# Performance work log

Hardware: AMD Instinct MI355X
Metric: run time of the kernel (lower is better)

Reference implementation:

```python
import jax, jax.numpy as jnp
import numpy as np

# YOLOv1 loss constants (from init_kwargs)
S, B, C = 28, 2, 20
L_COORD, L_NOOBJ = 5.0, 0.5
LEN_PRED = 5 * B + C  # 30
BS = 512


def setup_inputs() -> dict:
    key = jax.random.key(0)
    k1, k2, k3 = jax.random.split(key, 3)
    prediction = jax.random.uniform(k1, (BS, S, S, LEN_PRED), dtype=jnp.float32)
    target = jax.random.uniform(k2, (BS, S, S, LEN_PRED), dtype=jnp.float32)
    obj = jax.random.bernoulli(k3, 0.05, (BS, S, S)).astype(jnp.float32)
    idx = jnp.arange(LEN_PRED)
    is_conf = (idx < 5 * B) & (idx % 5 == 4)
    target = jnp.where(is_conf, obj[..., None], target)
    return {"prediction": prediction, "target": target}


def _xyxy(box):
    # [x, y, w, h] (cell-relative center, image-relative wh) -> [x1, y1, x2, y2]
    xy = box[..., :2] / S
    wh = box[..., 2:4]
    return xy - 0.5 * wh, xy + 0.5 * wh


def reference(prediction, target):
    N = prediction.shape[0]
    dt = prediction.dtype
    coo = (target[..., 4] > 0).astype(dt)   # (bs,S,S) cells with an object
    noo = 1.0 - coo                          # cells without an object

    pb = prediction[..., :5 * B].reshape(prediction.shape[:3] + (B, 5))  # (bs,S,S,B,5)
    tb = target[..., :5 * B].reshape(target.shape[:3] + (B, 5))

    # IoU of each predicted box vs the (single) target box of the cell
    p_lt, p_rb = _xyxy(pb)                 # (bs,S,S,B,2)
    t_lt, t_rb = _xyxy(tb[..., 0, :])      # (bs,S,S,2)
    lt = jnp.maximum(p_lt, t_lt[..., None, :])
    rb = jnp.minimum(p_rb, t_rb[..., None, :])
    wh = jnp.clip(rb - lt, 0.0)
    inter = wh[..., 0] * wh[..., 1]        # (bs,S,S,B)
    area1 = jnp.prod(p_rb - p_lt, axis=-1)
    area2 = jnp.prod(t_rb - t_lt, axis=-1)[..., None]
    iou = jax.lax.stop_gradient(inter / (area1 + area2 - inter))  # .data in torch

    max_idx = jnp.argmax(iou, axis=-1)     # responsible box per cell
    max_iou = jnp.max(iou, axis=-1)
    resp = jax.nn.one_hot(max_idx, B, dtype=dt)    # (bs,S,S,B)
    w_resp = coo[..., None] * resp                  # responsible & object
    w_not = coo[..., None] * (1.0 - resp)           # not responsible & object

    # Term 1+2: location loss (xy MSE + sqrt-wh MSE) on responsible boxes
    d_xy = jnp.sum((pb[..., :2] - tb[..., :2]) ** 2, axis=-1)
    d_wh = jnp.sum((jnp.sqrt(pb[..., 2:4]) - jnp.sqrt(tb[..., 2:4])) ** 2, axis=-1)
    loc_loss = jnp.sum(w_resp * (d_xy + d_wh))

    contain_loss = jnp.sum(w_resp * (pb[..., 4] - max_iou[..., None]) ** 2)

    # Term 4a: not-responsible boxes in object cells -> confidence target 0
    not_response_loss = jnp.sum(w_not * pb[..., 4] ** 2)

    # Term 4b: confidence loss in no-object cells (all B boxes)
    nooobj_loss = jnp.sum(noo[..., None] * (pb[..., 4] - tb[..., 4]) ** 2)

    # Term 5: class MSE in object cells
    class_loss = jnp.sum(coo[..., None] * (prediction[..., 5 * B:] - target[..., 5 * B:]) ** 2)

    loss = (L_COORD * loc_loss + contain_loss
            + L_NOOBJ * (not_response_loss + nooobj_loss) + class_loss)
    return loss / N
```

## Files before the change

### kernel.cpp

```cpp
#include <hip/hip_runtime.h>

namespace {
constexpr int   kS          = 28;
constexpr int   kBatch      = 512;
constexpr int   kCells      = kBatch * kS * kS;
constexpr int   kTPB        = 256;
constexpr int   kTileCells  = 256;
constexpr int   kTileF      = kTileCells * 30;
constexpr int   kNBlocks    = kCells / kTileCells;
constexpr int   kChunks     = kTileF / (64 * 4);
constexpr float kLCoord     = 5.0f;
constexpr float kLNoobj     = 0.5f;
constexpr float kInvS       = 1.0f / 28.0f;
constexpr float kInvN       = 1.0f / 512.0f;
}

__device__ __forceinline__ void async16(const float* g, float* l) {
    __builtin_amdgcn_global_load_lds(
        (const __attribute__((address_space(1))) void*)g,
        (__attribute__((address_space(3))) void*)l,
        16, 0, 0);
}

__device__ __forceinline__ float cell_loss(const float* p, const float* t) {
    const float coo = (t[4] > 0.0f) ? 1.0f : 0.0f;

    const float t_cx = t[0] * kInvS, t_cy = t[1] * kInvS;
    const float t_ltx = t_cx - 0.5f * t[2];
    const float t_lty = t_cy - 0.5f * t[3];
    const float t_rbx = t_cx + 0.5f * t[2];
    const float t_rby = t_cy + 0.5f * t[3];
    const float area2 = (t_rbx - t_ltx) * (t_rby - t_lty);

    float iou0 = 0.0f, iou1 = 0.0f;
    #pragma unroll
    for (int b = 0; b < 2; ++b) {
        const float* pb = p + 5 * b;
        const float p_cx = pb[0] * kInvS, p_cy = pb[1] * kInvS;
        const float p_ltx = p_cx - 0.5f * pb[2];
        const float p_lty = p_cy - 0.5f * pb[3];
        const float p_rbx = p_cx + 0.5f * pb[2];
        const float p_rby = p_cy + 0.5f * pb[3];
        const float ltx = fmaxf(p_ltx, t_ltx);
        const float lty = fmaxf(p_lty, t_lty);
        const float rbx = fminf(p_rbx, t_rbx);
        const float rby = fminf(p_rby, t_rby);
        const float w = fmaxf(rbx - ltx, 0.0f);
        const float h = fmaxf(rby - lty, 0.0f);
        const float inter = w * h;
        const float area1 = (p_rbx - p_ltx) * (p_rby - p_lty);
        const float iou = inter / (area1 + area2 - inter);
        if (b == 0) iou0 = iou; else iou1 = iou;
    }
    const int   max_idx = (iou1 > iou0) ? 1 : 0;
    const float max_iou = fmaxf(iou0, iou1);

    float loc = 0.0f, contain = 0.0f, notresp = 0.0f, nooobj = 0.0f;
    #pragma unroll
    for (int b = 0; b < 2; ++b) {
        const float* pb = p + 5 * b;
        const float* tb = t + 5 * b;
        const float dx = pb[0] - tb[0];
        const float dy = pb[1] - tb[1];
        const float d_xy = dx * dx + dy * dy;
        const float sw = sqrtf(pb[2]) - sqrtf(tb[2]);
        const float sh = sqrtf(pb[3]) - sqrtf(tb[3]);
        const float d_wh = sw * sw + sh * sh;
        const float resp   = (b == max_idx) ? 1.0f : 0.0f;
        const float w_resp = coo * resp;
        const float w_not  = coo * (1.0f - resp);
        loc += w_resp * (d_xy + d_wh);
        const float dc = pb[4] - max_iou;
        contain += w_resp * dc * dc;
        notresp += w_not * pb[4] * pb[4];
        const float dn = pb[4] - tb[4];
        nooobj += (1.0f - coo) * dn * dn;
    }

    float cls = 0.0f;
    #pragma unroll
    for (int j = 10; j < 30; ++j) {
        const float d = p[j] - t[j];
        cls += d * d;
    }
    cls *= coo;

    return kLCoord * loc + contain + kLNoobj * (notresp + nooobj) + cls;
}

template <bool USE_WS>
__global__ __launch_bounds__(kTPB) void yolo_loss_kernel(
        const float* __restrict__ pred,
        const float* __restrict__ targ,
        float* __restrict__ dst) {
    __shared__ float lp[kTileF];
    __shared__ float lt[kTileF];
    __shared__ float wsum[kTPB / 64];

    const int tid  = threadIdx.x;
    const int lane = tid & 63;
    const int wid  = tid >> 6;

    const float* gp = pred + (size_t)blockIdx.x * kTileF;
    const float* gt = targ + (size_t)blockIdx.x * kTileF;

    for (int c = wid; c < kChunks; c += kTPB / 64) {
        const int f = c * 256 + lane * 4;
        async16(gp + f, &lp[c * 256]);
        async16(gt + f, &lt[c * 256]);
    }
    __syncthreads();

    float local = cell_loss(&lp[tid * 30], &lt[tid * 30]);

    #pragma unroll
    for (int off = 32; off > 0; off >>= 1)
        local += __shfl_down(local, off, 64);

    if (lane == 0) wsum[wid] = local;
    __syncthreads();
    if (tid == 0) {
        const float s = wsum[0] + wsum[1] + wsum[2] + wsum[3];
        if (USE_WS) dst[blockIdx.x] = s;
        else        atomicAdd(dst, s * kInvN);
    }
}

__global__ __launch_bounds__(256) void reduce_kernel(
        const float* __restrict__ part, float* __restrict__ out) {
    __shared__ float wsum[4];
    float s = 0.0f;
    for (int i = threadIdx.x; i < kNBlocks; i += 256) s += part[i];
    #pragma unroll
    for (int off = 32; off > 0; off >>= 1)
        s += __shfl_down(s, off, 64);
    const int lane = threadIdx.x & 63;
    const int wid  = threadIdx.x >> 6;
    if (lane == 0) wsum[wid] = s;
    __syncthreads();
    if (threadIdx.x == 0)
        out[0] = (wsum[0] + wsum[1] + wsum[2] + wsum[3]) * kInvN;
}

__global__ void zero_out_kernel(float* __restrict__ out) {
    if (threadIdx.x == 0) out[0] = 0.0f;
}

extern "C" void kernel_launch(void* const* d_in, const int* in_sizes, int n_in,
                              void* d_out, int out_size, void* d_ws, size_t ws_size,
                              hipStream_t stream) {
    const float* pred = (const float*)d_in[0];
    const float* targ = (const float*)d_in[1];
    float* out = (float*)d_out;

    if (ws_size >= (size_t)kNBlocks * sizeof(float)) {
        float* part = (float*)d_ws;
        yolo_loss_kernel<true><<<kNBlocks, kTPB, 0, stream>>>(pred, targ, part);
        reduce_kernel<<<1, 256, 0, stream>>>(part, out);
    } else {
        zero_out_kernel<<<1, 64, 0, stream>>>(out);
        yolo_loss_kernel<false><<<kNBlocks, kTPB, 0, stream>>>(pred, targ, out);
    }
}
```

Measured before the change: 23.04 us.

## Use persistent 512-block grid with double-buffered async LDS staging

```diff
diff --git a/kernel.cpp b/kernel.cpp
--- a/kernel.cpp
+++ b/kernel.cpp
@@ -1,18 +1,17 @@
 #include <hip/hip_runtime.h>
 
 namespace {
-constexpr int   kS          = 28;
-constexpr int   kBatch      = 512;
-constexpr int   kCells      = kBatch * kS * kS;
-constexpr int   kTPB        = 256;
-constexpr int   kTileCells  = 256;
-constexpr int   kTileF      = kTileCells * 30;
-constexpr int   kNBlocks    = kCells / kTileCells;
-constexpr int   kChunks     = kTileF / (64 * 4);
-constexpr float kLCoord     = 5.0f;
-constexpr float kLNoobj     = 0.5f;
-constexpr float kInvS       = 1.0f / 28.0f;
-constexpr float kInvN       = 1.0f / 512.0f;
+constexpr int   kCells     = 512 * 28 * 28;
+constexpr int   kHalfCells = 128;
+constexpr int   kHalfF     = kHalfCells * 30;
+constexpr int   kNHalves   = kCells / kHalfCells;
+constexpr int   kNBlk      = 512;
+constexpr int   kBaseH     = kNHalves / kNBlk;
+constexpr int   kExtra     = kNHalves % kNBlk;
+constexpr float kLCoord    = 5.0f;
+constexpr float kLNoobj    = 0.5f;
+constexpr float kInvS      = 1.0f / 28.0f;
+constexpr float kInvN      = 1.0f / 512.0f;
 }
 
 __device__ __forceinline__ void async16(const float* g, float* l) {
@@ -21,6 +20,8 @@
         (__attribute__((address_space(3))) void*)l,
         16, 0, 0);
 }
+__device__ __forceinline__ void wait_vm15() { asm volatile("s_waitcnt vmcnt(15)" ::: "memory"); }
+__device__ __forceinline__ void wait_vm0()  { asm volatile("s_waitcnt vmcnt(0)"  ::: "memory"); }
 
 __device__ __forceinline__ float cell_loss(const float* p, const float* t) {
     const float coo = (t[4] > 0.0f) ? 1.0f : 0.0f;
@@ -89,39 +90,57 @@
 }
 
 template <bool USE_WS>
-__global__ __launch_bounds__(kTPB) void yolo_loss_kernel(
+__global__ __launch_bounds__(128) void yolo_loss_kernel(
         const float* __restrict__ pred,
         const float* __restrict__ targ,
         float* __restrict__ dst) {
-    __shared__ float lp[kTileF];
-    __shared__ float lt[kTileF];
-    __shared__ float wsum[kTPB / 64];
+    __shared__ float lp[2][kHalfF];
+    __shared__ float lt[2][kHalfF];
+    __shared__ float wsum[2];
 
     const int tid  = threadIdx.x;
     const int lane = tid & 63;
     const int wid  = tid >> 6;
+    const int b    = blockIdx.x;
 
-    const float* gp = pred + (size_t)blockIdx.x * kTileF;
-    const float* gt = targ + (size_t)blockIdx.x * kTileF;
+    const int h0 = b * kBaseH + min(b, kExtra);
+    const int H  = kBaseH + (b < kExtra ? 1 : 0);
 
-    for (int c = wid; c < kChunks; c += kTPB / 64) {
-        const int f = c * 256 + lane * 4;
-        async16(gp + f, &lp[c * 256]);
-        async16(gt + f, &lt[c * 256]);
+    const float* gsrc = (wid == 0) ? pred : targ;
+
+    auto stage = [&](int h, int buf) {
+        const float* g = gsrc + (size_t)h * kHalfF;
+        float* l = (wid == 0) ? &lp[buf][0] : &lt[buf][0];
+        #pragma unroll
+        for (int c = 0; c < 15; ++c) {
+            const int f = c * 256 + lane * 4;
+            async16(g + f, l + c * 256);
+        }
+    };
+
+    stage(h0, 0);
+    if (H > 1) stage(h0 + 1, 1);
+
+    float acc = 0.0f;
+    for (int i = 0; i < H; ++i) {
+        const int buf = i & 1;
+        if (i + 1 < H) wait_vm15(); else wait_vm0();
+        __builtin_amdgcn_s_barrier();
+        acc += cell_loss(&lp[buf][tid * 30], &lt[buf][tid * 30]);
+        if (i + 2 < H) {
+            __builtin_amdgcn_s_barrier();
+            stage(h0 + i + 2, buf);
+        }
     }
-    __syncthreads();
-
-    float local = cell_loss(&lp[tid * 30], &lt[tid * 30]);
 
     #pragma unroll
     for (int off = 32; off > 0; off >>= 1)
-        local += __shfl_down(local, off, 64);
-
-    if (lane == 0) wsum[wid] = local;
+        acc += __shfl_down(acc, off, 64);
+    if (lane == 0) wsum[wid] = acc;
     __syncthreads();
     if (tid == 0) {
-        const float s = wsum[0] + wsum[1] + wsum[2] + wsum[3];
-        if (USE_WS) dst[blockIdx.x] = s;
+        const float s = wsum[0] + wsum[1];
+        if (USE_WS) dst[b] = s;
         else        atomicAdd(dst, s * kInvN);
     }
 }
@@ -130,7 +149,7 @@
         const float* __restrict__ part, float* __restrict__ out) {
     __shared__ float wsum[4];
     float s = 0.0f;
-    for (int i = threadIdx.x; i < kNBlocks; i += 256) s += part[i];
+    for (int i = threadIdx.x; i < kNBlk; i += 256) s += part[i];
     #pragma unroll
     for (int off = 32; off > 0; off >>= 1)
         s += __shfl_down(s, off, 64);
@@ -153,12 +172,12 @@
     const float* targ = (const float*)d_in[1];
     float* out = (float*)d_out;
 
-    if (ws_size >= (size_t)kNBlocks * sizeof(float)) {
+    if (ws_size >= (size_t)kNBlk * sizeof(float)) {
         float* part = (float*)d_ws;
-        yolo_loss_kernel<true><<<kNBlocks, kTPB, 0, stream>>>(pred, targ, part);
+        yolo_loss_kernel<true><<<kNBlk, 128, 0, stream>>>(pred, targ, part);
         reduce_kernel<<<1, 256, 0, stream>>>(part, out);
     } else {
         zero_out_kernel<<<1, 64, 0, stream>>>(out);
-        yolo_loss_kernel<false><<<kNBlocks, kTPB, 0, stream>>>(pred, targ, out);
+        yolo_loss_kernel<false><<<kNBlk, 128, 0, stream>>>(pred, targ, out);
     }
 }
```

Result: no change. 23.43 us (+1.7%).
